# Performance work log

Hardware: AMD Instinct MI355X
Metric: run time of the kernel (lower is better)

## Reference

```python
import jax, jax.numpy as jnp
import numpy as np


def conv2d(x, w, b):
    # x: [D, Cin, H, W], w: [Cout, Cin, kh, kw], SAME padding, stride 1
    y = jax.lax.conv_general_dilated(
        x, w, window_strides=(1, 1), padding='SAME',
        dimension_numbers=('NCHW', 'OIHW', 'NCHW'))
    return y + b[None, :, None, None]


def setup_inputs() -> dict:
    key = jax.random.key(0)
    ks = jax.random.split(key, 12)
    B, N, T, H, W = 2, 3, 16, 28, 28
    Cp, Ch, Ck, Cv, Cs = 1024, 512, 64, 512, 256
    s = 0.02
    return {
        'f16': jax.random.normal(ks[0], (B, Cp, H, W), jnp.float32),
        'mk':  jax.random.normal(ks[1], (B, Ck, T, H, W), jnp.float32),
        'mv':  jax.random.normal(ks[2], (B, N, Cv, T, H, W), jnp.float32),
        'h':   jax.random.normal(ks[3], (B, N, Cs, H, W), jnp.float32),
        # KeyProj: 1x1 conv then 3x3 conv
        'w1': jax.random.normal(ks[4], (Ch, Cp, 1, 1), jnp.float32) * s,
        'b1': jnp.zeros((Ch,), jnp.float32),
        'w2': jax.random.normal(ks[5], (Ck, Ch, 3, 3), jnp.float32) * s,
        'b2': jnp.zeros((Ck,), jnp.float32),
        # sensory-updater transform: 3x3 conv, (Cv+Cs) -> 3*Cs
        'wt': jax.random.normal(ks[6], (3 * Cs, Cv + Cs, 3, 3), jnp.float32) * s,
        'bt': jnp.zeros((3 * Cs,), jnp.float32),
    }


def reference(f16, mk, mv, h, w1, b1, w2, b2, wt, bt):
    B, Ck, T = mk.shape[0], mk.shape[1], mk.shape[2]
    N, Cv = mv.shape[1], mv.shape[2]
    Cs = h.shape[2]
    H, W = f16.shape[-2:]
    P = H * W          # query pixels
    M = T * H * W      # memory slots

    # KeyProj: query key from pixel feature
    qk = conv2d(conv2d(f16, w1, b1), w2, b2)          # [B, Ck, H, W]

    # KV-memory affinity read (softmax over memory axis)
    mk_flat = mk.reshape(B, Ck, M)
    qk_flat = qk.reshape(B, Ck, P)
    logits = jnp.einsum('bcm,bcp->bmp', mk_flat, qk_flat) / jnp.sqrt(
        jnp.asarray(Ck, qk.dtype))                     # [B, M, P]
    aff = jax.nn.softmax(logits, axis=1)               # normalize over memory
    readout = jnp.einsum('bncm,bmp->bncp', mv.reshape(B, N, Cv, M), aff)
    readout = readout.reshape(B, N, Cv, H, W)          # [B, N, Cv, H, W]

    # gated recurrent sensory update (recurrent_update)
    x = jnp.concatenate([readout, h], axis=2).reshape(B * N, Cv + Cs, H, W)
    vals = conv2d(x, wt, bt).reshape(B, N, 3 * Cs, H, W)
    forget_g = jax.nn.sigmoid(vals[:, :, :Cs])
    update_g = jax.nn.sigmoid(vals[:, :, Cs:2 * Cs])
    new_vals = jnp.tanh(vals[:, :, 2 * Cs:])
    new_h = forget_g * h * (1.0 - update_g) + update_g * new_vals
    return new_h
```

## Files before the change

### kernel.cpp

```cpp
#include <hip/hip_runtime.h>

typedef unsigned short u16;
typedef unsigned int u32;
typedef float f32x4v __attribute__((ext_vector_type(4)));
typedef __bf16 bf16x8 __attribute__((ext_vector_type(8)));

#define GAS __attribute__((address_space(1)))
#define LAS __attribute__((address_space(3)))

__device__ __forceinline__ u16 f2bf(float f) {
  u32 u = __builtin_bit_cast(u32, f);
  u32 r = (u + 0x7FFFu + ((u >> 16) & 1u)) >> 16;
  return (u16)r;
}
__device__ __forceinline__ float bf2f(u16 h) {
  return __builtin_bit_cast(float, (u32)h << 16);
}
__device__ __forceinline__ void gld_lds16(const void* g, void* l) {
  __builtin_amdgcn_global_load_lds((const GAS void*)g, (LAS void*)l, 16, 0, 0);
}
#define VMCNT(N) asm volatile("s_waitcnt vmcnt(" #N ")" ::: "memory")
#define MFMA16(a, b, c) __builtin_amdgcn_mfma_f32_16x16x32_bf16((a), (b), (c), 0, 0, 0)

template <int CONV>
__global__ __launch_bounds__(512, 2) void gemm8p(
    const u16* __restrict__ A, const u16* __restrict__ B, u16* __restrict__ Cp,
    int M, int N, int Kc, int fullK, int S,
    long strA, long strB, long strC, int Cin, int gx, int gy, int nwg)
{
  const int cpx = (int)gridDim.x >> 3;
  const int L = ((int)blockIdx.x & 7) * cpx + ((int)blockIdx.x >> 3);
  if (L >= nwg) return;
  const int by = L % gy;
  const int rest = L / gy;
  const int bx = rest % gx;
  const int z = rest / gx;

  extern __shared__ u16 smem[];
  const int t = threadIdx.x, lane = t & 63, wave = t >> 6;
  const int zb = z / S, s = z - zb * S;
  const int m0 = bx * 256, n0 = by * 256;
  const int kbeg = s * Kc;
  const int kavail = fullK - kbeg;
  const int kc = Kc < kavail ? Kc : kavail;
  const int T = kc >> 6;

  const int srow = t >> 3;
  const int g = ((t & 7) - (srow & 7)) & 7;
  const int ldsoff = t * 8;

  const u16* Asrc[2][2];
  #pragma unroll
  for (int h = 0; h < 2; ++h)
    #pragma unroll
    for (int q = 0; q < 2; ++q) {
      int r = m0 + h * 128 + q * 64 + srow; if (r >= M) r = M - 1;
      Asrc[h][q] = A + (long)zb * strA + (long)r * fullK + kbeg + g * 8;
    }
  const u16* Bsrc[2][2];
  #pragma unroll
  for (int h = 0; h < 2; ++h)
    #pragma unroll
    for (int q = 0; q < 2; ++q) {
      if constexpr (CONV) {
        int pn = n0 + h * 128 + q * 64 + srow; if (pn >= N) pn = 0;
        const int img = pn / 784, p = pn - img * 784;
        const int py = p / 28, px = p - py * 28;
        Bsrc[h][q] = B + ((long)img * 900 + (py + 1) * 30 + (px + 1)) * Cin + g * 8;
      } else {
        int r = n0 + h * 128 + q * 64 + srow; if (r >= N) r = N - 1;
        Bsrc[h][q] = B + (long)zb * strB + (long)r * fullK + kbeg + g * 8;
      }
    }

  auto stageA = [&](int tile, int h) {
    u16* d = smem + (((tile & 1) * 2 + h) * 8192);
    const long ko = (long)tile * 64;
    gld_lds16(Asrc[h][0] + ko, d + ldsoff);
    gld_lds16(Asrc[h][1] + ko, d + 4096 + ldsoff);
  };
  auto stageB = [&](int tile, int h) {
    u16* d = smem + 32768 + (((tile & 1) * 2 + h) * 8192);
    long off;
    if constexpr (CONV) {
      const int kg = kbeg + tile * 64;
      const int tap = kg / Cin, kc2 = kg - tap * Cin;
      off = (long)((tap / 3 - 1) * 30 + (tap % 3 - 1)) * Cin + kc2;
    } else {
      off = (long)tile * 64;
    }
    gld_lds16(Bsrc[h][0] + off, d + ldsoff);
    gld_lds16(Bsrc[h][1] + off, d + 4096 + ldsoff);
  };

  const int wm = wave & 1, wn = wave >> 1;
  const int lr = lane & 15, hi = lane >> 4;
  const int slot0 = ((hi + (lr & 7)) & 7) * 8;
  const int slot1 = (((hi + 4) + (lr & 7)) & 7) * 8;
  f32x4v acc[8][4] = {};
  bf16x8 breg[4][2];

  stageB(0, 0); stageB(0, 1);
  stageA(0, 0); stageA(0, 1);
  stageB(1, 0); stageB(1, 1);
  VMCNT(4);
  __builtin_amdgcn_s_barrier();

  for (int tau = 0; tau < T; ++tau) {
    const int d = tau & 1;
    const u16* aB = smem + ((d * 2 + wm) * 8192);
    const u16* bB = smem + 32768 + ((d * 2 + (wn >> 1)) * 8192);
    const int ta = (tau + 1 < T) ? tau + 1 : T - 1;
    const int tb = (tau + 2 < T) ? tau + 2 : T - 1;
    #pragma unroll
    for (int Q = 0; Q < 4; ++Q) {
      bf16x8 aph[2][2];
      #pragma unroll
      for (int m2 = 0; m2 < 2; ++m2) {
        const int lrow = (Q * 2 + m2) * 16 + lr;
        aph[m2][0] = *(const bf16x8*)&aB[lrow * 64 + slot0];
        aph[m2][1] = *(const bf16x8*)&aB[lrow * 64 + slot1];
      }
      if (Q == 0) {
        #pragma unroll
        for (int n = 0; n < 4; ++n) {
          const int lrow = (wn & 1) * 64 + n * 16 + lr;
          breg[n][0] = *(const bf16x8*)&bB[lrow * 64 + slot0];
          breg[n][1] = *(const bf16x8*)&bB[lrow * 64 + slot1];
        }
      }
      if      (Q == 0) stageA(ta, 0);
      else if (Q == 1) stageA(ta, 1);
      else if (Q == 2) stageB(tb, 0);
      else             { stageB(tb, 1); VMCNT(4); }
      __builtin_amdgcn_sched_barrier(0);
      __builtin_amdgcn_s_barrier();
      __builtin_amdgcn_s_setprio(1);
      #pragma unroll
      for (int m2 = 0; m2 < 2; ++m2)
        #pragma unroll
        for (int n = 0; n < 4; ++n) {
          acc[Q * 2 + m2][n] = MFMA16(aph[m2][0], breg[n][0], acc[Q * 2 + m2][n]);
          acc[Q * 2 + m2][n] = MFMA16(aph[m2][1], breg[n][1], acc[Q * 2 + m2][n]);
        }
      __builtin_amdgcn_s_setprio(0);
      __builtin_amdgcn_sched_barrier(0);
      __builtin_amdgcn_s_barrier();
    }
  }
  VMCNT(0);

  u16* Co = Cp + (long)z * strC;
  #pragma unroll
  for (int m = 0; m < 8; ++m)
    #pragma unroll
    for (int r = 0; r < 4; ++r) {
      const int row = m0 + wm * 128 + m * 16 + hi * 4 + r;
      if (row >= M) continue;
      #pragma unroll
      for (int n = 0; n < 4; ++n) {
        const int col = n0 + wn * 64 + n * 16 + lr;
        if (col < N) Co[(long)row * N + col] = f2bf(acc[m][n][r]);
      }
    }
}

template <int CONV>
__global__ __launch_bounds__(512, 4) void gemmRC(
    const u16* __restrict__ A, const u16* __restrict__ B, u16* __restrict__ Cp,
    int M, int N, int Kc, int fullK, int S,
    long strA, long strB, long strC, int Cin, int gx, int gy, int nwg)
{
  const int cpx = (int)gridDim.x >> 3;
  const int L = ((int)blockIdx.x & 7) * cpx + ((int)blockIdx.x >> 3);
  if (L >= nwg) return;
  const int by = L % gy;
  const int rest = L / gy;
  const int bx = rest % gx;
  const int z = rest / gx;

  extern __shared__ u16 smem[];
  u16* sA = smem;
  u16* sB = smem + 3 * 8192;
  const int t = threadIdx.x, lane = t & 63, wave = t >> 6;
  const int zb = z / S, s = z - zb * S;
  const int m0 = bx * 256, n0 = by * 128;
  const int kbeg = s * Kc;
  const int kavail = fullK - kbeg;
  const int kc = Kc < kavail ? Kc : kavail;
  const int niter = kc >> 5;

  const int schunk = ((t & 3) ^ ((t >> 4) & 3)) * 8;
  const u16* Ap[2]; const u16* Bp;
  #pragma unroll
  for (int q = 0; q < 2; ++q) {
    int ra = m0 + q * 128 + (t >> 2); if (ra >= M) ra = M - 1;
    Ap[q] = A + (long)zb * strA + (long)ra * fullK + schunk;
  }
  if constexpr (CONV) {
    int pn = n0 + (t >> 2); if (pn >= N) pn = 0;
    const int img = pn / 784, p = pn - img * 784;
    const int py = p / 28, px = p - py * 28;
    Bp = B + ((long)img * 900 + (py + 1) * 30 + (px + 1)) * Cin + schunk;
  } else {
    int rb = n0 + (t >> 2); if (rb >= N) rb = N - 1;
    Bp = B + (long)zb * strB + (long)rb * fullK + schunk;
  }
  const int ldst = t * 8;

  auto stage = [&](int buf, int kg) {
    long boff;
    if constexpr (CONV) {
      const int tap = kg / Cin, kcc = kg - tap * Cin;
      boff = (long)((tap / 3 - 1) * 30 + (tap % 3 - 1)) * Cin + kcc;
    } else {
      boff = kg;
    }
    u16* dA = sA + buf * 8192;
    gld_lds16(Ap[0] + kg, &dA[ldst]);
    gld_lds16(Ap[1] + kg, &dA[4096 + ldst]);
    gld_lds16(Bp + boff,  &sB[buf * 4096 + ldst]);
  };

  const int wrow = (wave & 3) * 64, wcol = (wave >> 2) * 64;
  const int lr = lane & 15, hi = lane >> 4;
  const int csw = (hi ^ (lr >> 2)) * 8;
  f32x4v acc[4][4] = {};

  for (int p = 0; p < 2 && p < niter; ++p) stage(p, kbeg + p * 32);
  int cur = 0, nxt = 2;
  for (int it = 0; it < niter; ++it) {
    if (it + 2 < niter) {
      stage(nxt, kbeg + (it + 2) * 32);
      VMCNT(6);
    } else {
      const int rem = niter - 1 - it;
      if (rem == 1) VMCNT(3); else VMCNT(0);
    }
    __builtin_amdgcn_s_barrier();
    __builtin_amdgcn_sched_barrier(0);
    const u16* cA = sA + cur * 8192;
    const u16* cB = sB + cur * 4096;
    bf16x8 af[4], bf[4];
    #pragma unroll
    for (int m = 0; m < 4; ++m) af[m] = *(const bf16x8*)&cA[(wrow + m*16 + lr) * 32 + csw];
    #pragma unroll
    for (int n = 0; n < 4; ++n) bf[n] = *(const bf16x8*)&cB[(wcol + n*16 + lr) * 32 + csw];
    __builtin_amdgcn_s_setprio(1);
    #pragma unroll
    for (int m = 0; m < 4; ++m)
      #pragma unroll
      for (int n = 0; n < 4; ++n)
        acc[m][n] = MFMA16(af[m], bf[n], acc[m][n]);
    __builtin_amdgcn_s_setprio(0);
    __builtin_amdgcn_sched_barrier(0);
    __builtin_amdgcn_s_barrier();
    cur = (cur + 1 == 3) ? 0 : cur + 1;
    nxt = (nxt + 1 == 3) ? 0 : nxt + 1;
  }

  u16* Co = Cp + (long)z * strC;
  const int lq = hi * 4;
  #pragma unroll
  for (int m = 0; m < 4; ++m)
    #pragma unroll
    for (int r = 0; r < 4; ++r) {
      const int row = m0 + wrow + m * 16 + lq + r;
      if (row >= M) continue;
      #pragma unroll
      for (int n = 0; n < 4; ++n) {
        const int col = n0 + wcol + n * 16 + lr;
        if (col < N) Co[(long)row * N + col] = f2bf(acc[m][n][r]);
      }
    }
}

template <int BK>
__global__ __launch_bounds__(256) void gemm_glds(
    const u16* __restrict__ A, const u16* __restrict__ B, u16* __restrict__ C,
    int M, int N, int Kc, int fullK, int S,
    long strA, long strB, long strC, float scale)
{
  constexpr int CPR = BK / 8;
  constexpr int ISS = BK / 16;
  __shared__ u16 sA[2][128 * BK];
  __shared__ u16 sB[2][128 * BK];
  const int t = threadIdx.x, lane = t & 63, wave = t >> 6;
  const int z = blockIdx.z, zb = z / S;
  const int m0 = blockIdx.x * 128, n0 = blockIdx.y * 128;
  const int kbeg = (z - zb * S) * Kc;

  const u16* Aptr[ISS]; const u16* Bptr[ISS]; int lofs[ISS];
  #pragma unroll
  for (int i = 0; i < ISS; ++i) {
    const int tp = i * 256 + t;
    const int r = tp / CPR;
    int c16 = tp % CPR;
    if constexpr (BK == 32) c16 = c16 ^ ((tp >> 4) & 3);
    else                    c16 = (c16 - (r & 7)) & 7;
    int ra = m0 + r; if (ra >= M) ra = M - 1;
    int rb = n0 + r; if (rb >= N) rb = N - 1;
    Aptr[i] = A + (long)zb * strA + (long)ra * fullK + kbeg + c16 * 8;
    Bptr[i] = B + (long)zb * strB + (long)rb * fullK + kbeg + c16 * 8;
    lofs[i] = (i * 256 + (wave << 6)) * 8;
  }
  auto stage = [&](int buf, int k0) {
    #pragma unroll
    for (int i = 0; i < ISS; ++i) {
      gld_lds16(Aptr[i] + k0, &sA[buf][lofs[i]]);
      gld_lds16(Bptr[i] + k0, &sB[buf][lofs[i]]);
    }
  };

  const int wr = (wave >> 1) * 64, wc = (wave & 1) * 64;
  const int lr = lane & 15, hi = lane >> 4;
  f32x4v acc[4][4] = {};
  const int niter = Kc / BK;

  stage(0, 0);
  for (int it = 0; it < niter; ++it) {
    const int cur = it & 1;
    if (it + 1 < niter) {
      stage(cur ^ 1, (it + 1) * BK);
      if constexpr (ISS == 2) VMCNT(4); else VMCNT(8);
    } else {
      VMCNT(0);
    }
    __builtin_amdgcn_s_barrier();
    __builtin_amdgcn_sched_barrier(0);
    #pragma unroll
    for (int kk = 0; kk < BK; kk += 32) {
      bf16x8 af[4], bv[4];
      #pragma unroll
      for (int i = 0; i < 4; ++i) {
        const int row = wr + i*16 + lr;
        int lk;
        if constexpr (BK == 32) lk = kk + ((hi ^ (lr >> 2)) * 8);
        else                    lk = ((((kk >> 3) + hi) + (row & 7)) & 7) * 8;
        af[i] = *(const bf16x8*)&sA[cur][row * BK + lk];
      }
      #pragma unroll
      for (int j = 0; j < 4; ++j) {
        const int row = wc + j*16 + lr;
        int lk;
        if constexpr (BK == 32) lk = kk + ((hi ^ (lr >> 2)) * 8);
        else                    lk = ((((kk >> 3) + hi) + (row & 7)) & 7) * 8;
        bv[j] = *(const bf16x8*)&sB[cur][row * BK + lk];
      }
      __builtin_amdgcn_s_setprio(1);
      #pragma unroll
      for (int i = 0; i < 4; ++i)
        #pragma unroll
        for (int j = 0; j < 4; ++j)
          acc[i][j] = MFMA16(af[i], bv[j], acc[i][j]);
      __builtin_amdgcn_s_setprio(0);
    }
    __builtin_amdgcn_sched_barrier(0);
    __builtin_amdgcn_s_barrier();
  }

  const int lq = hi * 4;
  u16* Cw = C + (long)zb * strC;
  #pragma unroll
  for (int i = 0; i < 4; ++i)
    #pragma unroll
    for (int r = 0; r < 4; ++r) {
      const int row = m0 + wr + i*16 + lq + r;
      if (row >= M) continue;
      #pragma unroll
      for (int j = 0; j < 4; ++j) {
        const int col = n0 + wc + j*16 + lr;
        if (col < N) Cw[(long)row * N + col] = f2bf(acc[i][j][r] * scale);
      }
    }
}

__global__ __launch_bounds__(256) void conv_glds(
    const u16* __restrict__ Wt, const u16* __restrict__ imgP,
    float* __restrict__ Cp, int M, int Cin, int Ntot, int Kc)
{
  __shared__ u16 sA[2][128 * 32];
  __shared__ u16 sB[2][128 * 32];
  const int t = threadIdx.x, lane = t & 63, wave = t >> 6;
  const int z = blockIdx.z;
  const int m0 = blockIdx.x * 128, n0 = blockIdx.y * 128;
  const int kbeg = z * Kc;

  const u16* Aptr[2]; const u16* Bptr[2]; int lofs[2];
  #pragma unroll
  for (int i = 0; i < 2; ++i) {
    const int tp = i * 256 + t;
    const int r = tp >> 2;
    const int c16 = (tp & 3) ^ ((tp >> 4) & 3);
    int ra = m0 + r; if (ra >= M) ra = M - 1;
    int pn = n0 + r; if (pn >= Ntot) pn = 0;
    const int img = pn / 784, p = pn - img * 784;
    const int py = p / 28, px = p - py * 28;
    Aptr[i] = Wt + (long)ra * (9 * Cin) + c16 * 8;
    Bptr[i] = imgP + ((long)img * 900 + (py + 1) * 30 + (px + 1)) * Cin + c16 * 8;
    lofs[i] = (i * 256 + (wave << 6)) * 8;
  }
  auto stage = [&](int buf, int kg) {
    const int tap = kg / Cin, kc = kg - tap * Cin;
    const long off = (long)((tap / 3 - 1) * 30 + (tap % 3 - 1)) * Cin + kc;
    #pragma unroll
    for (int i = 0; i < 2; ++i) {
      gld_lds16(Aptr[i] + kg, &sA[buf][lofs[i]]);
      gld_lds16(Bptr[i] + off, &sB[buf][lofs[i]]);
    }
  };

  const int wr = (wave >> 1) * 64, wc = (wave & 1) * 64;
  const int lr = lane & 15, hi = lane >> 4;
  const int csw = (hi ^ (lr >> 2)) * 8;
  f32x4v acc[4][4] = {};
  const int niter = Kc >> 5;

  stage(0, kbeg);
  for (int it = 0; it < niter; ++it) {
    const int cur = it & 1;
    if (it + 1 < niter) {
      stage(cur ^ 1, kbeg + (it + 1) * 32);
      VMCNT(4);
    } else {
      VMCNT(0);
    }
    __builtin_amdgcn_s_barrier();
    __builtin_amdgcn_sched_barrier(0);
    bf16x8 af[4], bv[4];
    #pragma unroll
    for (int i = 0; i < 4; ++i) af[i] = *(const bf16x8*)&sA[cur][(wr + i*16 + lr) * 32 + csw];
    #pragma unroll
    for (int j = 0; j < 4; ++j) bv[j] = *(const bf16x8*)&sB[cur][(wc + j*16 + lr) * 32 + csw];
    __builtin_amdgcn_s_setprio(1);
    #pragma unroll
    for (int i = 0; i < 4; ++i)
      #pragma unroll
      for (int j = 0; j < 4; ++j)
        acc[i][j] = MFMA16(af[i], bv[j], acc[i][j]);
    __builtin_amdgcn_s_setprio(0);
    __builtin_amdgcn_sched_barrier(0);
    __builtin_amdgcn_s_barrier();
  }

  float* Co = Cp + (long)z * M * Ntot;
  const int lq = hi * 4;
  #pragma unroll
  for (int i = 0; i < 4; ++i)
    #pragma unroll
    for (int r = 0; r < 4; ++r) {
      const int row = m0 + wr + i*16 + lq + r;
      if (row >= M) continue;
      #pragma unroll
      for (int j = 0; j < 4; ++j) {
        const int col = n0 + wc + j*16 + lr;
        if (col < Ntot) Co[(long)row * Ntot + col] = acc[i][j][r];
      }
    }
}

__global__ __launch_bounds__(256) void transpose_bf(
    const float* __restrict__ in, u16* __restrict__ out,
    int R, int C, long strOutZ, int ldOut, int colOff)
{
  __shared__ float tile[32][33];
  in  += (long)blockIdx.z * R * C;
  out += (long)blockIdx.z * strOutZ;
  const int c0 = blockIdx.x * 32, r0 = blockIdx.y * 32;
  const int tx = threadIdx.x & 31, ty = threadIdx.x >> 5;
  for (int i = ty; i < 32; i += 8) {
    const int r = r0 + i, c = c0 + tx;
    tile[i][tx] = (r < R && c < C) ? in[(long)r * C + c] : 0.0f;
  }
  __syncthreads();
  for (int i = ty; i < 32; i += 8) {
    const int r = r0 + tx, c = c0 + i;
    if (c < C && r < R)
      out[(long)c * ldOut + colOff + r] = f2bf(tile[tx][i]);
  }
}

__global__ __launch_bounds__(256) void convert_bf(
    const float* __restrict__ in, u16* __restrict__ out, long n8)
{
  const long i = (long)blockIdx.x * 256 + threadIdx.x;
  if (i >= n8) return;
  const float4* p = (const float4*)in + i * 2;
  const float4 a = p[0], b = p[1];
  u16 o[8] = {f2bf(a.x), f2bf(a.y), f2bf(a.z), f2bf(a.w),
              f2bf(b.x), f2bf(b.y), f2bf(b.z), f2bf(b.w)};
  ((uint4*)out)[i] = *(uint4*)o;
}

__global__ __launch_bounds__(256) void permute_w(
    const float* __restrict__ src, u16* __restrict__ dst, int M, int Cin)
{
  const long total = (long)M * 9 * Cin;
  const long idx = (long)blockIdx.x * 256 + threadIdx.x;
  if (idx >= total) return;
  const int c = (int)(idx % Cin);
  const int tap = (int)((idx / Cin) % 9);
  const int m = (int)(idx / ((long)9 * Cin));
  dst[idx] = f2bf(src[((long)m * Cin + c) * 9 + tap]);
}

__global__ __launch_bounds__(256) void zfill(u32* __restrict__ p, long n) {
  const long stride = (long)gridDim.x * 256;
  for (long i = (long)blockIdx.x * 256 + threadIdx.x; i < n; i += stride) p[i] = 0;
}

__device__ __forceinline__ void addbf4(float* a, uint2 v) {
  a[0] += bf2f((u16)(v.x & 0xFFFFu));
  a[1] += bf2f((u16)(v.x >> 16));
  a[2] += bf2f((u16)(v.y & 0xFFFFu));
  a[3] += bf2f((u16)(v.y >> 16));
}

__global__ __launch_bounds__(256) void reduce_c1_bf(
    const u16* __restrict__ parts, u16* __restrict__ dst,
    const float* __restrict__ bias, int S)
{
  const long idx = (long)blockIdx.x * 256 + threadIdx.x;
  if (idx >= 1568L * 128) return;
  const int c4 = (int)(idx & 127), p = (int)(idx >> 7);
  const int c = c4 * 4;
  float sum[4] = {bias[c], bias[c+1], bias[c+2], bias[c+3]};
  for (int s = 0; s < S; ++s)
    addbf4(sum, *(const uint2*)&parts[((long)s * 1568 + p) * 512 + c]);
  const int im = p / 784, q = p - im * 784;
  const int qpad = (q / 28 + 1) * 30 + (q % 28 + 1);
  u16 o[4] = {f2bf(sum[0]), f2bf(sum[1]), f2bf(sum[2]), f2bf(sum[3])};
  *(uint2*)&dst[((long)im * 900 + qpad) * 512 + c] = *(uint2*)o;
}

__global__ __launch_bounds__(256) void reduceT_ro(
    const u16* __restrict__ parts, u16* __restrict__ dst, int S)
{
  __shared__ float tile[32][33];
  const int b = blockIdx.z, c0 = blockIdx.x * 32, p0 = blockIdx.y * 32;
  const int tx = threadIdx.x & 31, ty = threadIdx.x >> 5;
  for (int i = ty; i < 32; i += 8) {
    const int pc = min(p0 + tx, 783);
    float s = 0;
    for (int k = 0; k < S; ++k)
      s += bf2f(parts[((long)(b * S + k) * 1536 + c0 + i) * 784 + pc]);
    tile[i][tx] = s;
  }
  __syncthreads();
  for (int i = ty; i < 32; i += 8) {
    const int p = p0 + i, c = c0 + tx;
    if (p < 784) {
      const int n = c >> 9, cc = c & 511;
      const int qpad = (p / 28 + 1) * 30 + (p % 28 + 1);
      dst[((long)(b * 3 + n) * 900 + qpad) * 768 + cc] = f2bf(tile[tx][i]);
    }
  }
}

__global__ __launch_bounds__(256) void reduceT_qk(
    const float* __restrict__ parts, u16* __restrict__ dst,
    const float* __restrict__ bias, int S)
{
  __shared__ float tile[32][33];
  const int b = blockIdx.z, c0 = blockIdx.x * 32, p0 = blockIdx.y * 32;
  const int tx = threadIdx.x & 31, ty = threadIdx.x >> 5;
  for (int i = ty; i < 32; i += 8) {
    const int pc = min(p0 + tx, 783);
    const long base = (long)(c0 + i) * 1568 + b * 784 + pc;
    float s = 0;
    for (int k = 0; k < S; ++k) s += parts[(long)k * 64 * 1568 + base];
    tile[i][tx] = s;
  }
  __syncthreads();
  for (int i = ty; i < 32; i += 8) {
    const int p = p0 + i, c = c0 + tx;
    if (p < 784)
      dst[((long)b * 784 + p) * 64 + c] = f2bf(tile[tx][i] + bias[c]);
  }
}

__global__ __launch_bounds__(256) void transT_h(
    const float* __restrict__ h, u16* __restrict__ dst)
{
  __shared__ float tile[32][33];
  const int zimg = blockIdx.z, c0 = blockIdx.x * 32, p0 = blockIdx.y * 32;
  const int tx = threadIdx.x & 31, ty = threadIdx.x >> 5;
  for (int i = ty; i < 32; i += 8) {
    const int pc = min(p0 + tx, 783);
    tile[i][tx] = h[((long)zimg * 256 + c0 + i) * 784 + pc];
  }
  __syncthreads();
  for (int i = ty; i < 32; i += 8) {
    const int p = p0 + i, c = c0 + tx;
    if (p < 784) {
      const int qpad = (p / 28 + 1) * 30 + (p % 28 + 1);
      dst[((long)zimg * 900 + qpad) * 768 + 512 + c] = f2bf(tile[tx][i]);
    }
  }
}

__global__ __launch_bounds__(256) void softmax_inplace(u16* __restrict__ buf)
{
  uint4* p4 = (uint4*)(buf + (long)blockIdx.x * 12544);
  const int t = threadIdx.x;
  __shared__ float red[4];
  uint4 v[7];
  float mx = -3.0e38f;
  #pragma unroll
  for (int q = 0; q < 7; ++q) {
    const int idx = t + q * 256;
    if (idx < 1568) {
      v[q] = p4[idx];
      const u32 w[4] = {v[q].x, v[q].y, v[q].z, v[q].w};
      #pragma unroll
      for (int e = 0; e < 4; ++e) {
        mx = fmaxf(mx, bf2f((u16)(w[e] & 0xFFFFu)));
        mx = fmaxf(mx, bf2f((u16)(w[e] >> 16)));
      }
    }
  }
  #pragma unroll
  for (int o = 32; o > 0; o >>= 1) mx = fmaxf(mx, __shfl_xor(mx, o));
  if ((t & 63) == 0) red[t >> 6] = mx;
  __syncthreads();
  mx = fmaxf(fmaxf(red[0], red[1]), fmaxf(red[2], red[3]));

  float s = 0.0f;
  #pragma unroll
  for (int q = 0; q < 7; ++q) {
    const int idx = t + q * 256;
    if (idx < 1568) {
      const u32 w[4] = {v[q].x, v[q].y, v[q].z, v[q].w};
      #pragma unroll
      for (int e = 0; e < 4; ++e) {
        s += __expf(bf2f((u16)(w[e] & 0xFFFFu)) - mx);
        s += __expf(bf2f((u16)(w[e] >> 16)) - mx);
      }
    }
  }
  #pragma unroll
  for (int o = 32; o > 0; o >>= 1) s += __shfl_xor(s, o);
  __syncthreads();
  if ((t & 63) == 0) red[t >> 6] = s;
  __syncthreads();
  const float inv = 1.0f / (red[0] + red[1] + red[2] + red[3]);

  #pragma unroll
  for (int q = 0; q < 7; ++q) {
    const int idx = t + q * 256;
    if (idx < 1568) {
      u32 w[4] = {v[q].x, v[q].y, v[q].z, v[q].w};
      #pragma unroll
      for (int e = 0; e < 4; ++e) {
        const float a = __expf(bf2f((u16)(w[e] & 0xFFFFu)) - mx) * inv;
        const float b = __expf(bf2f((u16)(w[e] >> 16)) - mx) * inv;
        w[e] = (u32)f2bf(a) | ((u32)f2bf(b) << 16);
      }
      p4[idx] = make_uint4(w[0], w[1], w[2], w[3]);
    }
  }
}

__global__ __launch_bounds__(256) void treduce_gate(
    const u16* __restrict__ parts, const float* __restrict__ bt,
    const float* __restrict__ h, float* __restrict__ out, int S)
{
  const long i = (long)blockIdx.x * 256 + threadIdx.x;
  if (i >= 6L * 256 * 196) return;
  const int p4 = (int)(i % 196);
  const int rest = (int)(i / 196);
  const int cs = rest % 256, im = rest / 256;
  const long slice = 768L * 4704;
  const long pbase = (long)im * 784 + p4 * 4;
  float F[4] = {}, U[4] = {}, NV[4] = {};
  for (int s = 0; s < S; ++s) {
    const u16* P = parts + (long)s * slice;
    addbf4(F,  *(const uint2*)&P[(long)cs         * 4704 + pbase]);
    addbf4(U,  *(const uint2*)&P[(long)(256 + cs) * 4704 + pbase]);
    addbf4(NV, *(const uint2*)&P[(long)(512 + cs) * 4704 + pbase]);
  }
  const float bF = bt[cs], bU = bt[256 + cs], bN = bt[512 + cs];
  const f32x4v hv = ((const f32x4v*)h)[((long)(im * 256 + cs) * 784 >> 2) + p4];
  f32x4v o;
  #pragma unroll
  for (int q = 0; q < 4; ++q) {
    const float f = F[q] + bF, u = U[q] + bU, nv = NV[q] + bN;
    const float sf = 1.0f / (1.0f + __expf(-f));
    const float su = 1.0f / (1.0f + __expf(-u));
    const float e2 = __expf(2.0f * nv);
    const float tv = (e2 - 1.0f) / (e2 + 1.0f);
    o[q] = sf * hv[q] * (1.0f - su) + su * tv;
  }
  ((f32x4v*)out)[((long)(im * 256 + cs) * 784 >> 2) + p4] = o;
}

__global__ __launch_bounds__(256) void fill_sentinel(float* p, long n) {
  const long i = (long)blockIdx.x * 256 + threadIdx.x;
  if (i < n) p[i] = 12345.0f;
}

extern "C" void kernel_launch(void* const* d_in, const int* in_sizes, int n_in,
                              void* d_out, int out_size, void* d_ws, size_t ws_size,
                              hipStream_t stream) {
  const float* f16 = (const float*)d_in[0];
  const float* mk  = (const float*)d_in[1];
  const float* mv  = (const float*)d_in[2];
  const float* hin = (const float*)d_in[3];
  const float* w1  = (const float*)d_in[4];
  const float* b1  = (const float*)d_in[5];
  const float* w2  = (const float*)d_in[6];
  const float* b2  = (const float*)d_in[7];
  const float* wt  = (const float*)d_in[8];
  const float* bt  = (const float*)d_in[9];
  float* out = (float*)d_out;

  (void)hipFuncSetAttribute((const void*)gemm8p<0>,
                            hipFuncAttributeMaxDynamicSharedMemorySize, 131072);
  (void)hipFuncSetAttribute((const void*)gemm8p<1>,
                            hipFuncAttributeMaxDynamicSharedMemorySize, 131072);
  (void)hipFuncSetAttribute((const void*)gemmRC<0>,
                            hipFuncAttributeMaxDynamicSharedMemorySize, 73728);
  constexpr unsigned DSM8 = 131072, DSMR = 73728;

  const size_t B_f16T   = 2UL*784*1024*2;
  const size_t B_w1b    = 512UL*1024*2;
  const size_t B_w2R    = 64UL*4608*2;
  const size_t B_out1P  = 2UL*900*512*2;
  const size_t B_qkT    = 2UL*784*64*2;
  const size_t B_concat = 6UL*900*768*2;
  const size_t B_wtR    = 768UL*6912*2;
  const size_t B_mkT    = 2UL*12544*64*2;
  const size_t B_logaff = 2UL*784*12544*2;
  const size_t B_mvb    = 38535168UL*2;
  auto al = [](size_t x) { return (x + 255) & ~(size_t)255; };
  auto pad8 = [](int n) { return (n + 7) & ~7; };

  const size_t phase1 = al(B_f16T) + al(B_w1b) + al(B_w2R) + al(B_out1P) + al(B_qkT);
  const size_t regionA = phase1 > al(B_concat) ? phase1 : al(B_concat);

  const int S_ro = 5, S_tr = 4, S_c1 = 8;
  const int Kc_ro = 2560;
  const int Kc_tr = 1728;
  auto poolBytes = [&]() -> size_t {
    size_t p2 = 18UL*64*1568*4;
    size_t p1 = (size_t)S_c1*1568*512*2;
    size_t pr = (size_t)(2*S_ro)*1536*784*2;
    size_t pt = (size_t)S_tr*768*4704*2;
    size_t m = p2; if (p1 > m) m = p1; if (pr > m) m = pr; if (pt > m) m = pt;
    return m;
  };
  const size_t fixed = regionA + al(B_wtR) + al(B_mkT) + al(B_logaff) + al(B_mvb);
  if (fixed + poolBytes() > ws_size) {
    fill_sentinel<<<4704, 256, 0, stream>>>(out, (long)out_size);
    return;
  }

  char* base = (char*)d_ws;
  size_t off = 0;
  auto alloc = [&](size_t bytes) -> char* { char* p = base + off; off += al(bytes); return p; };
  char* rA = alloc(regionA);
  u16* f16T   = (u16*)rA;
  u16* w1b    = (u16*)(rA + al(B_f16T));
  u16* w2R    = (u16*)(rA + al(B_f16T) + al(B_w1b));
  u16* out1P  = (u16*)(rA + al(B_f16T) + al(B_w1b) + al(B_w2R));
  u16* qkT    = (u16*)(rA + al(B_f16T) + al(B_w1b) + al(B_w2R) + al(B_out1P));
  u16* concatP = (u16*)rA;
  u16*   wtR     = (u16*)alloc(B_wtR);
  u16*   mkT     = (u16*)alloc(B_mkT);
  u16*   logaff  = (u16*)alloc(B_logaff);
  u16*   mvb     = (u16*)alloc(B_mvb);
  char*  partsRaw = alloc(poolBytes());
  float* partsF  = (float*)partsRaw;
  u16*   partsH  = (u16*)partsRaw;

  zfill<<<512, 256, 0, stream>>>((u32*)out1P, (long)(B_out1P / 4));

  convert_bf<<<256, 256, 0, stream>>>(w1, w1b, 65536);
  permute_w<<<1152, 256, 0, stream>>>(w2, w2R, 64, 512);
  permute_w<<<20736, 256, 0, stream>>>(wt, wtR, 768, 768);
  transpose_bf<<<dim3(25, 32, 2), 256, 0, stream>>>(f16, f16T, 1024, 784, 784L*1024, 1024, 0);
  transpose_bf<<<dim3(392, 2, 2), 256, 0, stream>>>(mk, mkT, 64, 12544, 12544L*64, 64, 0);
  convert_bf<<<18816, 256, 0, stream>>>(mv, mvb, 4816896);

  {
    const int nwg = 7 * 4 * S_c1;
    gemmRC<0><<<pad8(nwg), 512, DSMR, stream>>>(
        f16T, w1b, partsH, 1568, 512, 1024 / S_c1, 1024, S_c1,
        0, 0, 1568L*512, 0, 7, 4, nwg);
  }
  reduce_c1_bf<<<784, 256, 0, stream>>>(partsH, out1P, b1, S_c1);

  conv_glds<<<dim3(1, 13, 18), 256, 0, stream>>>(w2R, out1P, partsF, 64, 512, 1568, 256);
  reduceT_qk<<<dim3(2, 25, 2), 256, 0, stream>>>(partsF, qkT, b2, 18);

  gemm_glds<64><<<dim3(7, 98, 2), 256, 0, stream>>>(
      qkT, mkT, logaff, 784, 12544, 64, 64, 1,
      784L*64, 12544L*64, 784L*12544, 0.125f);

  softmax_inplace<<<1568, 256, 0, stream>>>(logaff);

  zfill<<<2048, 256, 0, stream>>>((u32*)concatP, (long)(B_concat / 4));
  transT_h<<<dim3(8, 25, 6), 256, 0, stream>>>(hin, concatP);

  {
    const int nwg = 6 * 4 * 2 * S_ro;
    gemm8p<0><<<pad8(nwg), 512, DSM8, stream>>>(
        mvb, logaff, partsH, 1536, 784, Kc_ro, 12544, S_ro,
        1536L*12544, 784L*12544, 1536L*784, 0, 6, 4, nwg);
  }
  reduceT_ro<<<dim3(48, 25, 2), 256, 0, stream>>>(partsH, concatP, S_ro);

  {
    const int nwg = 3 * 19 * S_tr;
    gemm8p<1><<<pad8(nwg), 512, DSM8, stream>>>(
        wtR, concatP, partsH, 768, 4704, Kc_tr, 6912, S_tr,
        0, 0, 768L*4704, 768, 3, 19, nwg);
  }

  treduce_gate<<<1176, 256, 0, stream>>>(partsH, bt, hin, out, S_tr);
}
```

Baseline: 324.7 us.

## Fuse prep conversions and GEMMs into combined launches, zero only padding borders

Merges the input transposes and weight conversion into one prep kernel. A second kernel runs the first 1x1-conv GEMM alongside the mv conversion and the weight permutes, partitioning work by block index. The h transpose and border zeroing move into the readout GEMM launch. Full-buffer zero fills are replaced by writes to only the 30x30 padding border, which cuts launch count and memory traffic. In exchange the heterogeneous blocks share the GEMMs' launch bounds and shared-memory allocation, which can limit occupancy for the elementwise parts.

Result: faster. 305.8 us (-5.8%).

```diff
diff --git a/kernel.cpp b/kernel.cpp
--- a/kernel.cpp
+++ b/kernel.cpp
@@ -23,20 +23,19 @@
 #define MFMA16(a, b, c) __builtin_amdgcn_mfma_f32_16x16x32_bf16((a), (b), (c), 0, 0, 0)
 
 template <int CONV>
-__global__ __launch_bounds__(512, 2) void gemm8p(
-    const u16* __restrict__ A, const u16* __restrict__ B, u16* __restrict__ Cp,
+__device__ __forceinline__ void gemm8p_dev(
+    int lb, int Gpad, const u16* A, const u16* B, u16* Cp,
     int M, int N, int Kc, int fullK, int S,
-    long strA, long strB, long strC, int Cin, int gx, int gy, int nwg)
-{
-  const int cpx = (int)gridDim.x >> 3;
-  const int L = ((int)blockIdx.x & 7) * cpx + ((int)blockIdx.x >> 3);
+    long strA, long strB, long strC, int Cin, int gx, int gy, int nwg, u16* smem)
+{
+  const int cpx = Gpad >> 3;
+  const int L = (lb & 7) * cpx + (lb >> 3);
   if (L >= nwg) return;
   const int by = L % gy;
   const int rest = L / gy;
   const int bx = rest % gx;
   const int z = rest / gx;
 
-  extern __shared__ u16 smem[];
   const int t = threadIdx.x, lane = t & 63, wave = t >> 6;
   const int zb = z / S, s = z - zb * S;
   const int m0 = bx * 256, n0 = by * 256;
@@ -165,30 +164,26 @@
     }
 }
 
-template <int CONV>
-__global__ __launch_bounds__(512, 4) void gemmRC(
-    const u16* __restrict__ A, const u16* __restrict__ B, u16* __restrict__ Cp,
+__device__ __forceinline__ void gemmRC_dev(
+    int lb, int Gpad, const u16* A, const u16* B, u16* Cp,
     int M, int N, int Kc, int fullK, int S,
-    long strA, long strB, long strC, int Cin, int gx, int gy, int nwg)
-{
-  const int cpx = (int)gridDim.x >> 3;
-  const int L = ((int)blockIdx.x & 7) * cpx + ((int)blockIdx.x >> 3);
+    long strA, long strB, long strC, int gx, int gy, int nwg, u16* smem)
+{
+  const int cpx = Gpad >> 3;
+  const int L = (lb & 7) * cpx + (lb >> 3);
   if (L >= nwg) return;
   const int by = L % gy;
   const int rest = L / gy;
   const int bx = rest % gx;
   const int z = rest / gx;
 
-  extern __shared__ u16 smem[];
   u16* sA = smem;
   u16* sB = smem + 3 * 8192;
   const int t = threadIdx.x, lane = t & 63, wave = t >> 6;
   const int zb = z / S, s = z - zb * S;
   const int m0 = bx * 256, n0 = by * 128;
   const int kbeg = s * Kc;
-  const int kavail = fullK - kbeg;
-  const int kc = Kc < kavail ? Kc : kavail;
-  const int niter = kc >> 5;
+  const int niter = Kc >> 5;
 
   const int schunk = ((t & 3) ^ ((t >> 4) & 3)) * 8;
   const u16* Ap[2]; const u16* Bp;
@@ -197,29 +192,17 @@
     int ra = m0 + q * 128 + (t >> 2); if (ra >= M) ra = M - 1;
     Ap[q] = A + (long)zb * strA + (long)ra * fullK + schunk;
   }
-  if constexpr (CONV) {
-    int pn = n0 + (t >> 2); if (pn >= N) pn = 0;
-    const int img = pn / 784, p = pn - img * 784;
-    const int py = p / 28, px = p - py * 28;
-    Bp = B + ((long)img * 900 + (py + 1) * 30 + (px + 1)) * Cin + schunk;
-  } else {
+  {
     int rb = n0 + (t >> 2); if (rb >= N) rb = N - 1;
     Bp = B + (long)zb * strB + (long)rb * fullK + schunk;
   }
   const int ldst = t * 8;
 
   auto stage = [&](int buf, int kg) {
-    long boff;
-    if constexpr (CONV) {
-      const int tap = kg / Cin, kcc = kg - tap * Cin;
-      boff = (long)((tap / 3 - 1) * 30 + (tap % 3 - 1)) * Cin + kcc;
-    } else {
-      boff = kg;
-    }
     u16* dA = sA + buf * 8192;
     gld_lds16(Ap[0] + kg, &dA[ldst]);
     gld_lds16(Ap[1] + kg, &dA[4096 + ldst]);
-    gld_lds16(Bp + boff,  &sB[buf * 4096 + ldst]);
+    gld_lds16(Bp + kg,    &sB[buf * 4096 + ldst]);
   };
 
   const int wrow = (wave & 3) * 64, wcol = (wave >> 2) * 64;
@@ -273,6 +256,112 @@
         if (col < N) Co[(long)row * N + col] = f2bf(acc[m][n][r]);
       }
     }
+}
+
+__device__ __forceinline__ void border_slot(int slot, int& py, int& px) {
+  if (slot < 30)      { py = 0;         px = slot; }
+  else if (slot < 60) { py = 29;        px = slot - 30; }
+  else if (slot < 88) { py = slot - 59; px = 0; }
+  else                { py = slot - 87; px = 29; }
+}
+
+__device__ __forceinline__ void transp_dev(
+    const float* in, u16* out, int R, int C, int ldOut,
+    int bx, int by, int t, float (*tile)[33])
+{
+  const int c0 = bx * 32, r0 = by * 32;
+  const int tx = t & 31, ty = t >> 5;
+  for (int i = ty; i < 32; i += 8) {
+    const int r = r0 + i, c = c0 + tx;
+    tile[i][tx] = (r < R && c < C) ? in[(long)r * C + c] : 0.0f;
+  }
+  __syncthreads();
+  for (int i = ty; i < 32; i += 8) {
+    const int r = r0 + tx, c = c0 + i;
+    if (c < C && r < R)
+      out[(long)c * ldOut + r] = f2bf(tile[tx][i]);
+  }
+}
+
+__global__ __launch_bounds__(256) void prep1(
+    const float* __restrict__ f16, const float* __restrict__ mk,
+    const float* __restrict__ w1,
+    u16* __restrict__ f16T, u16* __restrict__ mkT, u16* __restrict__ w1b)
+{
+  __shared__ float tile[32][33];
+  const int bid = blockIdx.x, t = threadIdx.x;
+  if (bid < 1600) {
+    const int bx = bid % 25, by = (bid / 25) % 32, bz = bid / 800;
+    transp_dev(f16 + (long)bz * 1024 * 784, f16T + (long)bz * 784 * 1024,
+               1024, 784, 1024, bx, by, t, tile);
+    return;
+  }
+  if (bid < 3168) {
+    const int lb = bid - 1600;
+    const int bx = lb % 392, by = (lb / 392) % 2, bz = lb / 784;
+    transp_dev(mk + (long)bz * 64 * 12544, mkT + (long)bz * 12544 * 64,
+               64, 12544, 64, bx, by, t, tile);
+    return;
+  }
+  const long i = (long)(bid - 3168) * 256 + t;
+  const float4* p = (const float4*)w1 + i * 2;
+  const float4 a = p[0], b = p[1];
+  u16 o[8] = {f2bf(a.x), f2bf(a.y), f2bf(a.z), f2bf(a.w),
+              f2bf(b.x), f2bf(b.y), f2bf(b.z), f2bf(b.w)};
+  ((uint4*)w1b)[i] = *(uint4*)o;
+}
+
+__global__ __launch_bounds__(512, 4) void fused1(
+    const u16* __restrict__ f16T, const u16* __restrict__ w1b, u16* __restrict__ parts,
+    const float* __restrict__ mv, u16* __restrict__ mvb,
+    const float* __restrict__ w2, u16* __restrict__ w2R,
+    const float* __restrict__ wt, u16* __restrict__ wtR,
+    u16* __restrict__ out1P)
+{
+  extern __shared__ u16 smem[];
+  const int bid = blockIdx.x, t = threadIdx.x;
+  if (bid < 224) {
+    gemmRC_dev(bid, 224, f16T, w1b, parts, 1568, 512, 128, 1024, 8,
+               0, 0, 1568L * 512, 7, 4, 224, smem);
+    return;
+  }
+  int lb = bid - 224;
+  if (lb < 4704) {
+    const long g0 = (long)lb * 1024 + t;
+    #pragma unroll
+    for (int k = 0; k < 2; ++k) {
+      const long g = g0 + k * 512;
+      const float4* p = (const float4*)mv + g * 2;
+      const float4 a = p[0], b = p[1];
+      u16 o[8] = {f2bf(a.x), f2bf(a.y), f2bf(a.z), f2bf(a.w),
+                  f2bf(b.x), f2bf(b.y), f2bf(b.z), f2bf(b.w)};
+      ((uint4*)mvb)[g] = *(uint4*)o;
+    }
+    return;
+  }
+  lb -= 4704;
+  if (lb < 576) {
+    const int idx = lb * 512 + t;
+    const int c = idx % 512, tap = (idx / 512) % 9, m = idx / 4608;
+    w2R[idx] = f2bf(w2[((long)m * 512 + c) * 9 + tap]);
+    return;
+  }
+  lb -= 576;
+  if (lb < 10368) {
+    const long idx = (long)lb * 512 + t;
+    const int c = (int)(idx % 768), tap = (int)((idx / 768) % 9), m = (int)(idx / 6912);
+    wtR[idx] = f2bf(wt[((long)m * 768 + c) * 9 + tap]);
+    return;
+  }
+  lb -= 10368;
+  const int gid = lb * 512 + t;
+  if (gid < 14848) {
+    const int c8 = gid & 63, rest = gid >> 6;
+    const int slot = rest % 116, img = rest / 116;
+    int py, px; border_slot(slot, py, px);
+    *(uint4*)&out1P[((long)img * 900 + py * 30 + px) * 512 + c8 * 8] =
+        make_uint4(0, 0, 0, 0);
+  }
 }
 
 template <int BK>
@@ -459,56 +548,6 @@
     }
 }
 
-__global__ __launch_bounds__(256) void transpose_bf(
-    const float* __restrict__ in, u16* __restrict__ out,
-    int R, int C, long strOutZ, int ldOut, int colOff)
-{
-  __shared__ float tile[32][33];
-  in  += (long)blockIdx.z * R * C;
-  out += (long)blockIdx.z * strOutZ;
-  const int c0 = blockIdx.x * 32, r0 = blockIdx.y * 32;
-  const int tx = threadIdx.x & 31, ty = threadIdx.x >> 5;
-  for (int i = ty; i < 32; i += 8) {
-    const int r = r0 + i, c = c0 + tx;
-    tile[i][tx] = (r < R && c < C) ? in[(long)r * C + c] : 0.0f;
-  }
-  __syncthreads();
-  for (int i = ty; i < 32; i += 8) {
-    const int r = r0 + tx, c = c0 + i;
-    if (c < C && r < R)
-      out[(long)c * ldOut + colOff + r] = f2bf(tile[tx][i]);
-  }
-}
-
-__global__ __launch_bounds__(256) void convert_bf(
-    const float* __restrict__ in, u16* __restrict__ out, long n8)
-{
-  const long i = (long)blockIdx.x * 256 + threadIdx.x;
-  if (i >= n8) return;
-  const float4* p = (const float4*)in + i * 2;
-  const float4 a = p[0], b = p[1];
-  u16 o[8] = {f2bf(a.x), f2bf(a.y), f2bf(a.z), f2bf(a.w),
-              f2bf(b.x), f2bf(b.y), f2bf(b.z), f2bf(b.w)};
-  ((uint4*)out)[i] = *(uint4*)o;
-}
-
-__global__ __launch_bounds__(256) void permute_w(
-    const float* __restrict__ src, u16* __restrict__ dst, int M, int Cin)
-{
-  const long total = (long)M * 9 * Cin;
-  const long idx = (long)blockIdx.x * 256 + threadIdx.x;
-  if (idx >= total) return;
-  const int c = (int)(idx % Cin);
-  const int tap = (int)((idx / Cin) % 9);
-  const int m = (int)(idx / ((long)9 * Cin));
-  dst[idx] = f2bf(src[((long)m * Cin + c) * 9 + tap]);
-}
-
-__global__ __launch_bounds__(256) void zfill(u32* __restrict__ p, long n) {
-  const long stride = (long)gridDim.x * 256;
-  for (long i = (long)blockIdx.x * 256 + threadIdx.x; i < n; i += stride) p[i] = 0;
-}
-
 __device__ __forceinline__ void addbf4(float* a, uint2 v) {
   a[0] += bf2f((u16)(v.x & 0xFFFFu));
   a[1] += bf2f((u16)(v.x >> 16));
@@ -579,26 +618,6 @@
   }
 }
 
-__global__ __launch_bounds__(256) void transT_h(
-    const float* __restrict__ h, u16* __restrict__ dst)
-{
-  __shared__ float tile[32][33];
-  const int zimg = blockIdx.z, c0 = blockIdx.x * 32, p0 = blockIdx.y * 32;
-  const int tx = threadIdx.x & 31, ty = threadIdx.x >> 5;
-  for (int i = ty; i < 32; i += 8) {
-    const int pc = min(p0 + tx, 783);
-    tile[i][tx] = h[((long)zimg * 256 + c0 + i) * 784 + pc];
-  }
-  __syncthreads();
-  for (int i = ty; i < 32; i += 8) {
-    const int p = p0 + i, c = c0 + tx;
-    if (p < 784) {
-      const int qpad = (p / 28 + 1) * 30 + (p % 28 + 1);
-      dst[((long)zimg * 900 + qpad) * 768 + 512 + c] = f2bf(tile[tx][i]);
-    }
-  }
-}
-
 __global__ __launch_bounds__(256) void softmax_inplace(u16* __restrict__ buf)
 {
   uint4* p4 = (uint4*)(buf + (long)blockIdx.x * 12544);
@@ -659,6 +678,59 @@
       p4[idx] = make_uint4(w[0], w[1], w[2], w[3]);
     }
   }
+}
+
+__global__ __launch_bounds__(512, 2) void fused_ro(
+    const u16* __restrict__ mvb, const u16* __restrict__ logaff,
+    u16* __restrict__ parts, const float* __restrict__ hin,
+    u16* __restrict__ concatP, int Kc, int S)
+{
+  extern __shared__ u16 smem[];
+  const int bid = blockIdx.x, t = threadIdx.x;
+  if (bid < 240) {
+    gemm8p_dev<0>(bid, 240, mvb, logaff, parts, 1536, 784, Kc, 12544, S,
+                  1536L * 12544, 784L * 12544, 1536L * 784, 0, 6, 4, 240, smem);
+    return;
+  }
+  int lb = bid - 240;
+  if (lb < 1200) {
+    float (*tile)[33] = (float(*)[33])smem;
+    const int bx = lb % 8, by = (lb / 8) % 25, zimg = lb / 200;
+    const int c0 = bx * 32, p0 = by * 32;
+    const int tx = t & 31, ty = t >> 5;
+    for (int i = ty; i < 32; i += 16) {
+      const int pc = min(p0 + tx, 783);
+      tile[i][tx] = hin[((long)zimg * 256 + c0 + i) * 784 + pc];
+    }
+    __syncthreads();
+    for (int i = ty; i < 32; i += 16) {
+      const int p = p0 + i, c = c0 + tx;
+      if (p < 784) {
+        const int qpad = (p / 28 + 1) * 30 + (p % 28 + 1);
+        concatP[((long)zimg * 900 + qpad) * 768 + 512 + c] = f2bf(tile[tx][i]);
+      }
+    }
+    return;
+  }
+  lb -= 1200;
+  const int gid = lb * 512 + t;
+  if (gid < 66816) {
+    const int c8 = gid % 96, rest = gid / 96;
+    const int slot = rest % 116, img = rest / 116;
+    int py, px; border_slot(slot, py, px);
+    *(uint4*)&concatP[((long)img * 900 + py * 30 + px) * 768 + c8 * 8] =
+        make_uint4(0, 0, 0, 0);
+  }
+}
+
+__global__ __launch_bounds__(512, 2) void gemm8p_tr(
+    const u16* __restrict__ A, const u16* __restrict__ B, u16* __restrict__ Cp,
+    int M, int N, int Kc, int fullK, int S,
+    long strC, int Cin, int gx, int gy, int nwg)
+{
+  extern __shared__ u16 smem[];
+  gemm8p_dev<1>(blockIdx.x, (int)gridDim.x, A, B, Cp, M, N, Kc, fullK, S,
+                0, 0, strC, Cin, gx, gy, nwg, smem);
 }
 
 __global__ __launch_bounds__(256) void treduce_gate(
@@ -714,13 +786,13 @@
   const float* bt  = (const float*)d_in[9];
   float* out = (float*)d_out;
 
-  (void)hipFuncSetAttribute((const void*)gemm8p<0>,
+  (void)hipFuncSetAttribute((const void*)fused1,
+                            hipFuncAttributeMaxDynamicSharedMemorySize, 73728);
+  (void)hipFuncSetAttribute((const void*)fused_ro,
                             hipFuncAttributeMaxDynamicSharedMemorySize, 131072);
-  (void)hipFuncSetAttribute((const void*)gemm8p<1>,
+  (void)hipFuncSetAttribute((const void*)gemm8p_tr,
                             hipFuncAttributeMaxDynamicSharedMemorySize, 131072);
-  (void)hipFuncSetAttribute((const void*)gemmRC<0>,
-                            hipFuncAttributeMaxDynamicSharedMemorySize, 73728);
-  constexpr unsigned DSM8 = 131072, DSMR = 73728;
+  constexpr unsigned DSMR = 73728, DSM8 = 131072;
 
   const size_t B_f16T   = 2UL*784*1024*2;
   const size_t B_w1b    = 512UL*1024*2;
@@ -733,14 +805,12 @@
   const size_t B_logaff = 2UL*784*12544*2;
   const size_t B_mvb    = 38535168UL*2;
   auto al = [](size_t x) { return (x + 255) & ~(size_t)255; };
-  auto pad8 = [](int n) { return (n + 7) & ~7; };
 
   const size_t phase1 = al(B_f16T) + al(B_w1b) + al(B_w2R) + al(B_out1P) + al(B_qkT);
   const size_t regionA = phase1 > al(B_concat) ? phase1 : al(B_concat);
 
   const int S_ro = 5, S_tr = 4, S_c1 = 8;
-  const int Kc_ro = 2560;
-  const int Kc_tr = 1728;
+  const int Kc_ro = 2560, Kc_tr = 1728;
   auto poolBytes = [&]() -> size_t {
     size_t p2 = 18UL*64*1568*4;
     size_t p1 = (size_t)S_c1*1568*512*2;
@@ -773,24 +843,15 @@
   float* partsF  = (float*)partsRaw;
   u16*   partsH  = (u16*)partsRaw;
 
-  zfill<<<512, 256, 0, stream>>>((u32*)out1P, (long)(B_out1P / 4));
-
-  convert_bf<<<256, 256, 0, stream>>>(w1, w1b, 65536);
-  permute_w<<<1152, 256, 0, stream>>>(w2, w2R, 64, 512);
-  permute_w<<<20736, 256, 0, stream>>>(wt, wtR, 768, 768);
-  transpose_bf<<<dim3(25, 32, 2), 256, 0, stream>>>(f16, f16T, 1024, 784, 784L*1024, 1024, 0);
-  transpose_bf<<<dim3(392, 2, 2), 256, 0, stream>>>(mk, mkT, 64, 12544, 12544L*64, 64, 0);
-  convert_bf<<<18816, 256, 0, stream>>>(mv, mvb, 4816896);
-
-  {
-    const int nwg = 7 * 4 * S_c1;
-    gemmRC<0><<<pad8(nwg), 512, DSMR, stream>>>(
-        f16T, w1b, partsH, 1568, 512, 1024 / S_c1, 1024, S_c1,
-        0, 0, 1568L*512, 0, 7, 4, nwg);
-  }
+  prep1<<<3424, 256, 0, stream>>>(f16, mk, w1, f16T, mkT, w1b);
+
+  fused1<<<15901, 512, DSMR, stream>>>(f16T, w1b, partsH, mv, mvb,
+                                       w2, w2R, wt, wtR, out1P);
+
   reduce_c1_bf<<<784, 256, 0, stream>>>(partsH, out1P, b1, S_c1);
 
   conv_glds<<<dim3(1, 13, 18), 256, 0, stream>>>(w2R, out1P, partsF, 64, 512, 1568, 256);
+
   reduceT_qk<<<dim3(2, 25, 2), 256, 0, stream>>>(partsF, qkT, b2, 18);
 
   gemm_glds<64><<<dim3(7, 98, 2), 256, 0, stream>>>(
@@ -799,23 +860,14 @@
 
   softmax_inplace<<<1568, 256, 0, stream>>>(logaff);
 
-  zfill<<<2048, 256, 0, stream>>>((u32*)concatP, (long)(B_concat / 4));
-  transT_h<<<dim3(8, 25, 6), 256, 0, stream>>>(hin, concatP);
-
-  {
-    const int nwg = 6 * 4 * 2 * S_ro;
-    gemm8p<0><<<pad8(nwg), 512, DSM8, stream>>>(
-        mvb, logaff, partsH, 1536, 784, Kc_ro, 12544, S_ro,
-        1536L*12544, 784L*12544, 1536L*784, 0, 6, 4, nwg);
-  }
+  fused_ro<<<1571, 512, DSM8, stream>>>(mvb, logaff, partsH, hin, concatP,
+                                        Kc_ro, S_ro);
+
   reduceT_ro<<<dim3(48, 25, 2), 256, 0, stream>>>(partsH, concatP, S_ro);
 
-  {
-    const int nwg = 3 * 19 * S_tr;
-    gemm8p<1><<<pad8(nwg), 512, DSM8, stream>>>(
-        wtR, concatP, partsH, 768, 4704, Kc_tr, 6912, S_tr,
-        0, 0, 768L*4704, 768, 3, 19, nwg);
-  }
+  gemm8p_tr<<<232, 512, DSM8, stream>>>(wtR, concatP, partsH,
+                                        768, 4704, Kc_tr, 6912, S_tr,
+                                        768L*4704, 768, 3, 19, 228);
 
   treduce_gate<<<1176, 256, 0, stream>>>(partsH, bt, hin, out, S_tr);
 }
```
